# Kernel tuning notes

Hardware: AMD Instinct MI355X
Metric: run time of the kernel (lower is better)

Reference implementation:

```python
import jax, jax.numpy as jnp
import numpy as np

B, T, E = 2, 2048, 2048
H = 16
DH = E // H  # 128
FFN = 4 * E  # 8192
EPS = 1e-5


def _layernorm(x, g, b):
    mu = jnp.mean(x, axis=-1, keepdims=True)
    var = jnp.mean((x - mu) ** 2, axis=-1, keepdims=True)
    return (x - mu) * jax.lax.rsqrt(var + EPS) * g + b


def setup_inputs() -> dict:
    key = jax.random.key(0)
    ks = jax.random.split(key, 8)
    s = 0.02
    return {
        "x": jax.random.normal(ks[0], (B, T, E), jnp.float32),
        "g1": jnp.ones((E,), jnp.float32),
        "b1": jnp.zeros((E,), jnp.float32),
        "wq": jax.random.normal(ks[1], (E, E), jnp.float32) * s,
        "wk": jax.random.normal(ks[2], (E, E), jnp.float32) * s,
        "wv": jax.random.normal(ks[3], (E, E), jnp.float32) * s,
        "wo": jax.random.normal(ks[4], (E, E), jnp.float32) * s,
        "g2": jnp.ones((E,), jnp.float32),
        "b2": jnp.zeros((E,), jnp.float32),
        "w1": jax.random.normal(ks[5], (E, FFN), jnp.float32) * s,
        "w2": jax.random.normal(ks[6], (E, FFN), jnp.float32) * s,
        "w3": jax.random.normal(ks[7], (FFN, E), jnp.float32) * s,
    }


def reference(x, g1, b1, wq, wk, wv, wo, g2, b2, w1, w2, w3):
    Bx, Tx, Ex = x.shape
    # --- attention block (pre-LN, residual) ---
    h = _layernorm(x, g1, b1)
    q = (h @ wq).reshape(Bx, Tx, H, DH)
    k = (h @ wk).reshape(Bx, Tx, H, DH)
    v = (h @ wv).reshape(Bx, Tx, H, DH)
    scores = jnp.einsum('bqhd,bkhd->bhqk', q, k) / jnp.sqrt(jnp.float32(DH))
    causal = jnp.tril(jnp.ones((Tx, Tx), bool))  # [T,T]
    scores = jnp.where(causal[None, None], scores, -jnp.inf)
    attn = jax.nn.softmax(scores, axis=-1)
    ctx = jnp.einsum('bhqk,bkhd->bqhd', attn, v).reshape(Bx, Tx, H * DH)
    x = x + ctx @ wo
    # --- SwiGLU MLP block (pre-LN, residual) ---
    h = _layernorm(x, g2, b2)
    gated = jax.nn.silu(h @ w1) * (h @ w2)
    return x + gated @ w3
```

## Files before the change

kernel.cpp:

```cpp
#include <hip/hip_runtime.h>


#define T_SEQ 2048
#define E_DIM 2048
#define N_HEAD 16
#define D_HEAD 128
#define FFN_DIM 8192
#define M_ROWS 4096
#define QS (3 * E_DIM)

typedef unsigned short u16;
typedef short short8 __attribute__((ext_vector_type(8)));
typedef float f32x4 __attribute__((ext_vector_type(4)));

#define DEV __device__ __forceinline__

DEV u16 f2bf(float f) {
  unsigned u = __float_as_uint(f);
  u += 0x7fffu + ((u >> 16) & 1u);
  return (u16)(u >> 16);
}
DEV float bf2f(u16 h) { return __uint_as_float(((unsigned)h) << 16); }

DEV void async16(void* lds, const void* g) {
  __builtin_amdgcn_global_load_lds((const __attribute__((address_space(1))) void*)g,
                                   (__attribute__((address_space(3))) void*)lds, 16, 0, 0);
}

__global__ __launch_bounds__(256) void ln_kernel(const float* __restrict__ x,
                                                 const float* __restrict__ gw,
                                                 const float* __restrict__ bw,
                                                 u16* __restrict__ out) {
  int row = blockIdx.x;
  int t = threadIdx.x;
  const float4* xr = (const float4*)(x + (size_t)row * E_DIM);
  float4 a = xr[t], c = xr[t + 256];
  float s = a.x + a.y + a.z + a.w + c.x + c.y + c.z + c.w;
  float q = a.x * a.x + a.y * a.y + a.z * a.z + a.w * a.w +
            c.x * c.x + c.y * c.y + c.z * c.z + c.w * c.w;
  for (int off = 32; off > 0; off >>= 1) {
    s += __shfl_down(s, off);
    q += __shfl_down(q, off);
  }
  __shared__ float red[8];
  if ((t & 63) == 0) { red[(t >> 6) * 2] = s; red[(t >> 6) * 2 + 1] = q; }
  __syncthreads();
  s = red[0] + red[2] + red[4] + red[6];
  q = red[1] + red[3] + red[5] + red[7];
  float mu = s * (1.f / E_DIM);
  float rs = rsqrtf(q * (1.f / E_DIM) - mu * mu + 1e-5f);
  const float4* g4 = (const float4*)gw;
  const float4* b4 = (const float4*)bw;
  float4 g0 = g4[t], g1v = g4[t + 256], e0 = b4[t], e1 = b4[t + 256];
  ushort4 o0, o1;
  o0.x = f2bf((a.x - mu) * rs * g0.x + e0.x);
  o0.y = f2bf((a.y - mu) * rs * g0.y + e0.y);
  o0.z = f2bf((a.z - mu) * rs * g0.z + e0.z);
  o0.w = f2bf((a.w - mu) * rs * g0.w + e0.w);
  o1.x = f2bf((c.x - mu) * rs * g1v.x + e1.x);
  o1.y = f2bf((c.y - mu) * rs * g1v.y + e1.y);
  o1.z = f2bf((c.z - mu) * rs * g1v.z + e1.z);
  o1.w = f2bf((c.w - mu) * rs * g1v.w + e1.w);
  ((ushort4*)(out + (size_t)row * E_DIM))[t] = o0;
  ((ushort4*)(out + (size_t)row * E_DIM))[t + 256] = o1;
}

__global__ __launch_bounds__(256) void cvt_t_kernel(const float* __restrict__ W,
                                                    u16* __restrict__ WT,
                                                    int Kd, int Nd) {
  __shared__ float tile[32][33];
  int tx = threadIdx.x, ty = threadIdx.y;
  int n0 = blockIdx.x * 32, k0 = blockIdx.y * 32;
#pragma unroll
  for (int i = 0; i < 4; i++)
    tile[ty + i * 8][tx] = W[(size_t)(k0 + ty + i * 8) * Nd + n0 + tx];
  __syncthreads();
#pragma unroll
  for (int i = 0; i < 4; i++)
    WT[(size_t)(n0 + ty + i * 8) * Kd + k0 + tx] = f2bf(tile[tx][ty + i * 8]);
}

__global__ __launch_bounds__(256) void transpose_v_kernel(const u16* __restrict__ qkv,
                                                          u16* __restrict__ vt) {
  __shared__ u16 tile[32][33];
  int tx = threadIdx.x, ty = threadIdx.y;
  int b = blockIdx.z;
  int t0 = blockIdx.x * 32, e0 = blockIdx.y * 32;
#pragma unroll
  for (int i = 0; i < 4; i++)
    tile[ty + i * 8][tx] =
        qkv[(size_t)(b * T_SEQ + t0 + ty + i * 8) * QS + 2 * E_DIM + e0 + tx];
  __syncthreads();
#pragma unroll
  for (int i = 0; i < 4; i++)
    vt[((size_t)b * E_DIM + e0 + ty + i * 8) * T_SEQ + t0 + tx] = tile[tx][ty + i * 8];
}

template <int MODE, int BM_>
__global__ __launch_bounds__(512, 1) void gemm8p(const u16* __restrict__ A,
                                                 const u16* __restrict__ BT,
                                                 void* __restrict__ Cout,
                                                 const void* __restrict__ Extra,
                                                 int N, int K, int CX, int CY) {
  constexpr int MM = BM_ / 64;
  constexpr int AUNIT = BM_ * 32;
  __shared__ u16 Abuf[4 * AUNIT];
  __shared__ u16 Bbuf[4 * 8192];
  const int t = threadIdx.x;
  const int w = t >> 6, l = t & 63, g = l >> 4, lq = l & 15;
  const int wm = w >> 2, wn = w & 3;

  const int bid = blockIdx.y * gridDim.x + blockIdx.x;
  const int xcd = bid & 7, slot = bid >> 3;
  const int nchx = gridDim.x / CX;
  const int bx = (xcd % nchx) * CX + (slot % CX);
  const int by = (xcd / nchx) * CY + (slot / CX);
  const size_t bm = (size_t)by * BM_, bn = (size_t)bx * 256;

  const int srcrow = ((l >> 3) << 1) | (l & 1);
  const int csrc = ((((l >> 1) & 3) ^ ((l >> 3) & 3)) << 3);
  const u16* aSrc = A + (bm + w * 16 + srcrow) * (size_t)K + csrc;
  const u16* bSrc = BT + (bn + w * 16 + srcrow) * (size_t)K + csrc;
  const int rdoff = (((lq & 1) + 2 * (g ^ ((lq >> 1) & 3))) << 3);

#define STA8(DB, KS, TILE)                                                    \
  {                                                                           \
    u16* Ad = Abuf + (DB) * (2 * AUNIT) + (KS)*AUNIT + w * 512;               \
    const u16* as_ = aSrc + (size_t)(TILE)*64 + (KS)*32;                      \
    async16(Ad, as_);                                                         \
    if constexpr (BM_ == 256) async16(Ad + 4096, as_ + (size_t)128 * K);      \
  }
#define STB8(DB, KS, TILE)                                                    \
  {                                                                           \
    u16* Bd = Bbuf + (DB)*16384 + (KS)*8192 + w * 512;                        \
    const u16* bs_ = bSrc + (size_t)(TILE)*64 + (KS)*32;                      \
    async16(Bd, bs_);                                                         \
    async16(Bd + 4096, bs_ + (size_t)128 * K);                                \
  }
#define RDA8(DB, KS, MH)                                                      \
  _Pragma("unroll") for (int mm = 0; mm < MM; ++mm)                           \
      af[mm] = *(const short8*)(Abuf + (DB) * (2 * AUNIT) + (KS)*AUNIT +      \
                                (wm * (BM_ / 4) + (MH) * (BM_ / 8) + mm * 8 + \
                                 (lq >> 1)) * 64 + rdoff);
#define RDB8(DB, KS)                                                          \
  _Pragma("unroll") for (int nn = 0; nn < 4; ++nn)                            \
      bf[nn] = *(const short8*)(Bbuf + (DB)*16384 + (KS)*8192 +               \
                                (wn * 32 + nn * 8 + (lq >> 1)) * 64 + rdoff);
#define MM168(MH)                                                             \
  _Pragma("unroll") for (int mm = 0; mm < MM; ++mm)                           \
      _Pragma("unroll") for (int nn = 0; nn < 4; ++nn)                        \
          acc[(MH)*MM + mm][nn] = __builtin_amdgcn_mfma_f32_16x16x32_bf16(    \
              af[mm], bf[nn], acc[(MH)*MM + mm][nn], 0, 0, 0);
#define SYNCA                                                                 \
  __builtin_amdgcn_s_barrier();                                               \
  asm volatile("s_waitcnt lgkmcnt(0)" ::: "memory");                          \
  __builtin_amdgcn_sched_barrier(0);                                          \
  __builtin_amdgcn_s_setprio(1);
#define ENDP __builtin_amdgcn_s_setprio(0);
#define BAR2 __builtin_amdgcn_s_barrier();
#define WAITN                                                                 \
  if constexpr (BM_ == 256) asm volatile("s_waitcnt vmcnt(8)" ::: "memory");  \
  else                      asm volatile("s_waitcnt vmcnt(6)" ::: "memory");
#define WAITH                                                                 \
  if constexpr (BM_ == 256) asm volatile("s_waitcnt vmcnt(4)" ::: "memory");  \
  else                      asm volatile("s_waitcnt vmcnt(3)" ::: "memory");

  const int NT = K >> 6, NI = NT >> 1;
  f32x4 acc[2 * MM][4] = {};
  short8 af[MM > 4 ? MM : 4], bf[4];

  STA8(0, 0, 0); STB8(0, 0, 0);
  STA8(0, 1, 0); STB8(0, 1, 0);
  STA8(1, 0, 1); STB8(1, 0, 1);
  WAITN;
  BAR2;

  for (int j = 0; j < NI; ++j) {
    const int t1 = 2 * j + 1, t2 = 2 * j + 2, t3 = 2 * j + 3;
    const bool s2 = t2 < NT, s3 = t3 < NT, lastI = (j + 1 == NI);
    RDB8(0, 0); RDA8(0, 0, 0);
    STA8(1, 1, t1);
    SYNCA; MM168(0); ENDP; BAR2;
    RDA8(0, 0, 1);
    STB8(1, 1, t1);
    SYNCA; MM168(1); ENDP;
    WAITN;
    BAR2;
    RDB8(0, 1); RDA8(0, 1, 0);
    if (s2) STA8(0, 0, t2);
    SYNCA; MM168(0); ENDP; BAR2;
    RDA8(0, 1, 1);
    if (s2) STB8(0, 0, t2);
    SYNCA; MM168(1); ENDP;
    if (lastI) { WAITH; } else { WAITN; }
    BAR2;
    RDB8(1, 0); RDA8(1, 0, 0);
    if (s2) STA8(0, 1, t2);
    SYNCA; MM168(0); ENDP; BAR2;
    RDA8(1, 0, 1);
    if (s2) STB8(0, 1, t2);
    SYNCA; MM168(1); ENDP;
    if (lastI) { asm volatile("s_waitcnt vmcnt(0)" ::: "memory"); } else { WAITN; }
    BAR2;
    RDB8(1, 1); RDA8(1, 1, 0);
    if (s3) STA8(1, 0, t3);
    SYNCA; MM168(0); ENDP; BAR2;
    RDA8(1, 1, 1);
    if (s3) STB8(1, 0, t3);
    SYNCA; MM168(1); ENDP;
    if (!lastI) { WAITN; }
    BAR2;
  }
#undef STA8
#undef STB8
#undef RDA8
#undef RDB8
#undef MM168
#undef SYNCA
#undef ENDP
#undef BAR2
#undef WAITN
#undef WAITH

#pragma unroll
  for (int m = 0; m < 2 * MM; m++) {
    size_t row = bm + wm * (BM_ / 2) + m * 16 + 4 * g;
#pragma unroll
    for (int n = 0; n < 4; n++) {
      size_t col = bn + wn * 64 + n * 16 + lq;
#pragma unroll
      for (int r = 0; r < 4; r++) {
        size_t idx = (row + r) * (size_t)N + col;
        if constexpr (MODE == 0) {
          ((u16*)Cout)[idx] = f2bf(acc[m][n][r]);
        } else if constexpr (MODE == 1) {
          ((float*)Cout)[idx] = ((const float*)Extra)[idx] + acc[m][n][r];
        } else {
          float a = bf2f(((const u16*)Extra)[idx]);
          float sil = a / (1.f + exp2f(-1.4426950408889634f * a));
          ((u16*)Cout)[idx] = f2bf(sil * acc[m][n][r]);
        }
      }
    }
  }
}

__global__ __launch_bounds__(256, 3) void attn_kernel(const u16* __restrict__ QKV,
                                                      const u16* __restrict__ VT,
                                                      u16* __restrict__ CTX) {
  __shared__ u16 Ks[64 * 128];
  __shared__ u16 Vs[128 * 64];
  __shared__ u16 P_all[4][16 * 72];
  const int t = threadIdx.x;
  const int w = t >> 6, l = t & 63, g = l >> 4, lq = l & 15;
  u16* P = P_all[w];
  const int q0blk = blockIdx.x * 64;
  const int q0w = q0blk + w * 16;
  const int bh = blockIdx.y, b = bh >> 4, h = bh & 15;
  const u16* qp = QKV + (size_t)b * T_SEQ * QS + h * D_HEAD;
  const u16* kp = QKV + (size_t)b * T_SEQ * QS + E_DIM + h * D_HEAD;
  const u16* vp = VT + ((size_t)b * E_DIM + h * D_HEAD) * T_SEQ;

  short8 qf[4];
#pragma unroll
  for (int ks = 0; ks < 4; ks++)
    qf[ks] = *(const short8*)(qp + (size_t)(q0w + lq) * QS + ks * 32 + g * 8);

  f32x4 acc[8] = {};
  float m2[4], ls[4];
#pragma unroll
  for (int r = 0; r < 4; r++) { m2[r] = -1e30f; ls[r] = 0.f; }
  const float sc = 0.08838834764831845f * 1.4426950408889634f;

  const int kRow0 = 16 * w + (l >> 4);
  const int kChunk = l & 15;
  const int vRow0 = 32 * w + (l >> 3);
  const int vChunk = l & 7;

  for (int kv0 = 0; kv0 <= q0blk; kv0 += 64) {
#pragma unroll
    for (int j = 0; j < 4; j++) {
      int R = kRow0 + 4 * j;
      async16(Ks + (16 * w + 4 * j) * 128,
              kp + (size_t)(kv0 + R) * QS + ((kChunk ^ (R & 7)) << 3));
    }
#pragma unroll
    for (int j = 0; j < 4; j++) {
      int D = vRow0 + 8 * j;
      async16(Vs + (32 * w + 8 * j) * 64,
              vp + (size_t)D * T_SEQ + kv0 + ((vChunk ^ (D & 7)) << 3));
    }
    __syncthreads();

    f32x4 s[4];
#pragma unroll
    for (int ct = 0; ct < 4; ct++) {
      s[ct] = f32x4{0.f, 0.f, 0.f, 0.f};
#pragma unroll
      for (int ks = 0; ks < 4; ks++) {
        short8 kf = *(const short8*)(Ks + (ct * 16 + lq) * 128 +
                                     (((ks * 4 + g) ^ (lq & 7)) << 3));
        s[ct] = __builtin_amdgcn_mfma_f32_16x16x32_bf16(qf[ks], kf, s[ct], 0, 0, 0);
      }
    }
    float sv[4][4];
#pragma unroll
    for (int ct = 0; ct < 4; ct++)
#pragma unroll
      for (int r = 0; r < 4; r++) sv[ct][r] = s[ct][r] * sc;
    if (kv0 + 64 > q0w) {
#pragma unroll
      for (int ct = 0; ct < 4; ct++)
#pragma unroll
        for (int r = 0; r < 4; r++)
          if (kv0 + ct * 16 + lq > q0w + 4 * g + r) sv[ct][r] = -1e30f;
    }
    float mx[4];
#pragma unroll
    for (int r = 0; r < 4; r++)
      mx[r] = fmaxf(fmaxf(sv[0][r], sv[1][r]), fmaxf(sv[2][r], sv[3][r]));
#pragma unroll
    for (int off = 1; off < 16; off <<= 1)
#pragma unroll
      for (int r = 0; r < 4; r++) mx[r] = fmaxf(mx[r], __shfl_xor(mx[r], off));
#pragma unroll
    for (int r = 0; r < 4; r++) {
      float mn = fmaxf(m2[r], mx[r]);
      float sca = exp2f(m2[r] - mn);
      m2[r] = mn;
      float sum = 0.f;
#pragma unroll
      for (int ct = 0; ct < 4; ct++) {
        float pv = exp2f(sv[ct][r] - mn);
        sum += pv;
        P[(4 * g + r) * 72 + ct * 16 + lq] = f2bf(pv);
      }
      ls[r] = ls[r] * sca + sum;
#pragma unroll
      for (int n = 0; n < 8; n++) acc[n][r] *= sca;
    }
    short8 pa[2];
#pragma unroll
    for (int ks2 = 0; ks2 < 2; ks2++)
      pa[ks2] = *(const short8*)(P + lq * 72 + ks2 * 32 + g * 8);
#pragma unroll
    for (int n = 0; n < 8; n++)
#pragma unroll
      for (int ks2 = 0; ks2 < 2; ks2++) {
        short8 vf = *(const short8*)(Vs + (n * 16 + lq) * 64 +
                                     (((ks2 * 4 + g) ^ (lq & 7)) << 3));
        acc[n] = __builtin_amdgcn_mfma_f32_16x16x32_bf16(pa[ks2], vf, acc[n], 0, 0, 0);
      }
    __syncthreads();
  }

#pragma unroll
  for (int off = 1; off < 16; off <<= 1)
#pragma unroll
    for (int r = 0; r < 4; r++) ls[r] += __shfl_xor(ls[r], off);
  float inv[4];
#pragma unroll
  for (int r = 0; r < 4; r++) inv[r] = 1.f / ls[r];
  u16* cp = CTX + ((size_t)b * T_SEQ + q0w) * E_DIM + h * D_HEAD;
#pragma unroll
  for (int n = 0; n < 8; n++)
#pragma unroll
    for (int r = 0; r < 4; r++)
      cp[(size_t)(4 * g + r) * E_DIM + n * 16 + lq] = f2bf(acc[n][r] * inv[r]);
}

extern "C" void kernel_launch(void* const* d_in, const int* in_sizes, int n_in,
                              void* d_out, int out_size, void* d_ws, size_t ws_size,
                              hipStream_t stream) {
  (void)in_sizes; (void)n_in; (void)out_size; (void)ws_size;
  const float* x  = (const float*)d_in[0];
  const float* g1 = (const float*)d_in[1];
  const float* b1 = (const float*)d_in[2];
  const float* wq = (const float*)d_in[3];
  const float* wk = (const float*)d_in[4];
  const float* wv = (const float*)d_in[5];
  const float* wo = (const float*)d_in[6];
  const float* g2 = (const float*)d_in[7];
  const float* b2 = (const float*)d_in[8];
  const float* w1 = (const float*)d_in[9];
  const float* w2 = (const float*)d_in[10];
  const float* w3 = (const float*)d_in[11];
  float* out = (float*)d_out;

  const size_t EE2 = (size_t)E_DIM * E_DIM * 2;
  const size_t EF2 = (size_t)E_DIM * FFN_DIM * 2;
  const size_t ME2 = (size_t)M_ROWS * E_DIM * 2;
  char* p = (char*)d_ws;
  u16* wqkvT = (u16*)p; p += 3 * EE2;
  u16* woT = (u16*)p; p += EE2;
  u16* w1T = (u16*)p; p += EF2;
  u16* w2T = (u16*)p; p += EF2;
  u16* w3T = (u16*)p; p += EF2;
  u16* Hb  = (u16*)p; p += ME2;
  u16* QKVb = (u16*)p; p += (size_t)M_ROWS * QS * 2;
  u16* VTb = (u16*)p; p += ME2;
  u16* CTXb = (u16*)p; p += ME2;
  u16* U1b = QKVb;

  dim3 blk32(32, 8);
  cvt_t_kernel<<<dim3(E_DIM / 32, E_DIM / 32), blk32, 0, stream>>>(wq, wqkvT, E_DIM, E_DIM);
  cvt_t_kernel<<<dim3(E_DIM / 32, E_DIM / 32), blk32, 0, stream>>>(wk, wqkvT + E_DIM * E_DIM, E_DIM, E_DIM);
  cvt_t_kernel<<<dim3(E_DIM / 32, E_DIM / 32), blk32, 0, stream>>>(wv, wqkvT + 2 * E_DIM * E_DIM, E_DIM, E_DIM);
  cvt_t_kernel<<<dim3(E_DIM / 32, E_DIM / 32), blk32, 0, stream>>>(wo, woT, E_DIM, E_DIM);
  cvt_t_kernel<<<dim3(FFN_DIM / 32, E_DIM / 32), blk32, 0, stream>>>(w1, w1T, E_DIM, FFN_DIM);
  cvt_t_kernel<<<dim3(FFN_DIM / 32, E_DIM / 32), blk32, 0, stream>>>(w2, w2T, E_DIM, FFN_DIM);
  cvt_t_kernel<<<dim3(E_DIM / 32, FFN_DIM / 32), blk32, 0, stream>>>(w3, w3T, FFN_DIM, E_DIM);

  ln_kernel<<<M_ROWS, 256, 0, stream>>>(x, g1, b1, Hb);
  gemm8p<0, 128><<<dim3(QS / 256, M_ROWS / 128), 512, 0, stream>>>(Hb, wqkvT, QKVb, nullptr, QS, E_DIM, 6, 16);
  transpose_v_kernel<<<dim3(T_SEQ / 32, E_DIM / 32, 2), blk32, 0, stream>>>(QKVb, VTb);
  attn_kernel<<<dim3(T_SEQ / 64, 2 * N_HEAD), 256, 0, stream>>>(QKVb, VTb, CTXb);
  gemm8p<1, 128><<<dim3(E_DIM / 256, M_ROWS / 128), 512, 0, stream>>>(CTXb, woT, out, x, E_DIM, E_DIM, 4, 8);

  ln_kernel<<<M_ROWS, 256, 0, stream>>>(out, g2, b2, Hb);
  gemm8p<0, 256><<<dim3(FFN_DIM / 256, M_ROWS / 256), 512, 0, stream>>>(Hb, w1T, U1b, nullptr, FFN_DIM, E_DIM, 8, 8);
  gemm8p<2, 256><<<dim3(FFN_DIM / 256, M_ROWS / 256), 512, 0, stream>>>(Hb, w2T, U1b, U1b, FFN_DIM, E_DIM, 8, 8);
  gemm8p<1, 128><<<dim3(E_DIM / 256, M_ROWS / 128), 512, 0, stream>>>(U1b, w3T, out, out, E_DIM, FFN_DIM, 4, 8);
}
```

Measured before the change: 942.3 us.

## Split-K the down-projection GEMM and process 32 query rows per attention wave

The final FFN down-projection GEMM now uses 256-row tiles and a two-way split over K. Each half writes fp32 partials into the reused weight workspace, and a separate add kernel sums them into the residual output. This is meant to raise per-block work and parallelism for the long-K GEMM, at the cost of extra partial-sum memory traffic and one more launch. The attention kernel now handles 128 queries per block with two 16-row groups per wave, reusing each loaded K/V tile twice. It also adds MFMA priority hints and lowers occupancy to 2 blocks per CU.

```diff
diff --git a/kernel.cpp b/kernel.cpp
--- a/kernel.cpp
+++ b/kernel.cpp
@@ -96,12 +96,32 @@
     vt[((size_t)b * E_DIM + e0 + ty + i * 8) * T_SEQ + t0 + tx] = tile[tx][ty + i * 8];
 }
 
+__global__ __launch_bounds__(256) void add3_kernel(float* __restrict__ out,
+                                                   const float* __restrict__ pk) {
+  const size_t MN4 = (size_t)M_ROWS * E_DIM / 4;
+  size_t i = (size_t)blockIdx.x * 256 + threadIdx.x;
+  const float4* p04 = (const float4*)pk;
+  const float4* p14 = (const float4*)(pk + (size_t)M_ROWS * E_DIM);
+  float4* o4 = (float4*)out;
+#pragma unroll
+  for (int k = 0; k < 4; k++) {
+    size_t idx = i + (size_t)k * 524288;
+    if (idx < MN4) {
+      float4 o = o4[idx], a = p04[idx], b = p14[idx];
+      o.x += a.x + b.x; o.y += a.y + b.y;
+      o.z += a.z + b.z; o.w += a.w + b.w;
+      o4[idx] = o;
+    }
+  }
+}
+
 template <int MODE, int BM_>
 __global__ __launch_bounds__(512, 1) void gemm8p(const u16* __restrict__ A,
                                                  const u16* __restrict__ BT,
                                                  void* __restrict__ Cout,
                                                  const void* __restrict__ Extra,
-                                                 int N, int K, int CX, int CY) {
+                                                 int N, int K, int lda, int ldb,
+                                                 int CX, int CY) {
   constexpr int MM = BM_ / 64;
   constexpr int AUNIT = BM_ * 32;
   __shared__ u16 Abuf[4 * AUNIT];
@@ -110,17 +130,22 @@
   const int w = t >> 6, l = t & 63, g = l >> 4, lq = l & 15;
   const int wm = w >> 2, wn = w & 3;
 
-  const int bid = blockIdx.y * gridDim.x + blockIdx.x;
+  const int bid = (blockIdx.z * gridDim.y + blockIdx.y) * gridDim.x + blockIdx.x;
   const int xcd = bid & 7, slot = bid >> 3;
   const int nchx = gridDim.x / CX;
-  const int bx = (xcd % nchx) * CX + (slot % CX);
-  const int by = (xcd / nchx) * CY + (slot / CX);
+  const int nchy = gridDim.y / CY;
+  const int cpz = nchx * nchy;
+  const int kz = xcd / cpz;
+  const int cid = xcd % cpz;
+  const int bx = (cid % nchx) * CX + (slot % CX);
+  const int by = (cid / nchx) * CY + (slot / CX);
   const size_t bm = (size_t)by * BM_, bn = (size_t)bx * 256;
+  const size_t koff = (size_t)kz * K;
 
   const int srcrow = ((l >> 3) << 1) | (l & 1);
   const int csrc = ((((l >> 1) & 3) ^ ((l >> 3) & 3)) << 3);
-  const u16* aSrc = A + (bm + w * 16 + srcrow) * (size_t)K + csrc;
-  const u16* bSrc = BT + (bn + w * 16 + srcrow) * (size_t)K + csrc;
+  const u16* aSrc = A + (bm + w * 16 + srcrow) * (size_t)lda + koff + csrc;
+  const u16* bSrc = BT + (bn + w * 16 + srcrow) * (size_t)ldb + koff + csrc;
   const int rdoff = (((lq & 1) + 2 * (g ^ ((lq >> 1) & 3))) << 3);
 
 #define STA8(DB, KS, TILE)                                                    \
@@ -128,14 +153,14 @@
     u16* Ad = Abuf + (DB) * (2 * AUNIT) + (KS)*AUNIT + w * 512;               \
     const u16* as_ = aSrc + (size_t)(TILE)*64 + (KS)*32;                      \
     async16(Ad, as_);                                                         \
-    if constexpr (BM_ == 256) async16(Ad + 4096, as_ + (size_t)128 * K);      \
+    if constexpr (BM_ == 256) async16(Ad + 4096, as_ + (size_t)128 * lda);    \
   }
 #define STB8(DB, KS, TILE)                                                    \
   {                                                                           \
     u16* Bd = Bbuf + (DB)*16384 + (KS)*8192 + w * 512;                        \
     const u16* bs_ = bSrc + (size_t)(TILE)*64 + (KS)*32;                      \
     async16(Bd, bs_);                                                         \
-    async16(Bd + 4096, bs_ + (size_t)128 * K);                                \
+    async16(Bd + 4096, bs_ + (size_t)128 * ldb);                              \
   }
 #define RDA8(DB, KS, MH)                                                      \
   _Pragma("unroll") for (int mm = 0; mm < MM; ++mm)                           \
@@ -222,6 +247,7 @@
 #undef WAITN
 #undef WAITH
 
+  const size_t mn = (size_t)gridDim.y * BM_ * (size_t)N;
 #pragma unroll
   for (int m = 0; m < 2 * MM; m++) {
     size_t row = bm + wm * (BM_ / 2) + m * 16 + 4 * g;
@@ -235,41 +261,48 @@
           ((u16*)Cout)[idx] = f2bf(acc[m][n][r]);
         } else if constexpr (MODE == 1) {
           ((float*)Cout)[idx] = ((const float*)Extra)[idx] + acc[m][n][r];
-        } else {
+        } else if constexpr (MODE == 2) {
           float a = bf2f(((const u16*)Extra)[idx]);
           float sil = a / (1.f + exp2f(-1.4426950408889634f * a));
           ((u16*)Cout)[idx] = f2bf(sil * acc[m][n][r]);
+        } else {
+          ((float*)Cout)[(size_t)kz * mn + idx] = acc[m][n][r];
         }
       }
     }
   }
 }
 
-__global__ __launch_bounds__(256, 3) void attn_kernel(const u16* __restrict__ QKV,
+__global__ __launch_bounds__(256, 2) void attn_kernel(const u16* __restrict__ QKV,
                                                       const u16* __restrict__ VT,
                                                       u16* __restrict__ CTX) {
   __shared__ u16 Ks[64 * 128];
   __shared__ u16 Vs[128 * 64];
-  __shared__ u16 P_all[4][16 * 72];
+  __shared__ u16 P_all[4][32 * 72];
   const int t = threadIdx.x;
   const int w = t >> 6, l = t & 63, g = l >> 4, lq = l & 15;
   u16* P = P_all[w];
-  const int q0blk = blockIdx.x * 64;
-  const int q0w = q0blk + w * 16;
+  const int q0blk = blockIdx.x * 128;
+  const int q0w = q0blk + w * 32;
   const int bh = blockIdx.y, b = bh >> 4, h = bh & 15;
   const u16* qp = QKV + (size_t)b * T_SEQ * QS + h * D_HEAD;
   const u16* kp = QKV + (size_t)b * T_SEQ * QS + E_DIM + h * D_HEAD;
   const u16* vp = VT + ((size_t)b * E_DIM + h * D_HEAD) * T_SEQ;
 
-  short8 qf[4];
-#pragma unroll
-  for (int ks = 0; ks < 4; ks++)
-    qf[ks] = *(const short8*)(qp + (size_t)(q0w + lq) * QS + ks * 32 + g * 8);
-
-  f32x4 acc[8] = {};
-  float m2[4], ls[4];
-#pragma unroll
-  for (int r = 0; r < 4; r++) { m2[r] = -1e30f; ls[r] = 0.f; }
+  short8 qf[2][4];
+#pragma unroll
+  for (int rg = 0; rg < 2; rg++)
+#pragma unroll
+    for (int ks = 0; ks < 4; ks++)
+      qf[rg][ks] =
+          *(const short8*)(qp + (size_t)(q0w + rg * 16 + lq) * QS + ks * 32 + g * 8);
+
+  f32x4 acc[2][8] = {};
+  float m2[2][4], ls[2][4];
+#pragma unroll
+  for (int rg = 0; rg < 2; rg++)
+#pragma unroll
+    for (int r = 0; r < 4; r++) { m2[rg][r] = -1e30f; ls[rg][r] = 0.f; }
   const float sc = 0.08838834764831845f * 1.4426950408889634f;
 
   const int kRow0 = 16 * w + (l >> 4);
@@ -277,7 +310,7 @@
   const int vRow0 = 32 * w + (l >> 3);
   const int vChunk = l & 7;
 
-  for (int kv0 = 0; kv0 <= q0blk; kv0 += 64) {
+  for (int kv0 = 0; kv0 < q0blk + 128; kv0 += 64) {
 #pragma unroll
     for (int j = 0; j < 4; j++) {
       int R = kRow0 + 4 * j;
@@ -292,81 +325,97 @@
     }
     __syncthreads();
 
-    f32x4 s[4];
-#pragma unroll
-    for (int ct = 0; ct < 4; ct++) {
-      s[ct] = f32x4{0.f, 0.f, 0.f, 0.f};
-#pragma unroll
-      for (int ks = 0; ks < 4; ks++) {
-        short8 kf = *(const short8*)(Ks + (ct * 16 + lq) * 128 +
-                                     (((ks * 4 + g) ^ (lq & 7)) << 3));
-        s[ct] = __builtin_amdgcn_mfma_f32_16x16x32_bf16(qf[ks], kf, s[ct], 0, 0, 0);
+#pragma unroll
+    for (int rg = 0; rg < 2; rg++) {
+      const int rb = q0w + rg * 16;
+      if (kv0 > rb + 15) continue;
+      f32x4 s[4];
+      __builtin_amdgcn_s_setprio(1);
+#pragma unroll
+      for (int ct = 0; ct < 4; ct++) {
+        s[ct] = f32x4{0.f, 0.f, 0.f, 0.f};
+#pragma unroll
+        for (int ks = 0; ks < 4; ks++) {
+          short8 kf = *(const short8*)(Ks + (ct * 16 + lq) * 128 +
+                                       (((ks * 4 + g) ^ (lq & 7)) << 3));
+          s[ct] = __builtin_amdgcn_mfma_f32_16x16x32_bf16(qf[rg][ks], kf, s[ct], 0, 0, 0);
+        }
       }
+      __builtin_amdgcn_s_setprio(0);
+      float sv[4][4];
+#pragma unroll
+      for (int ct = 0; ct < 4; ct++)
+#pragma unroll
+        for (int r = 0; r < 4; r++) sv[ct][r] = s[ct][r] * sc;
+      if (kv0 + 64 > rb) {
+#pragma unroll
+        for (int ct = 0; ct < 4; ct++)
+#pragma unroll
+          for (int r = 0; r < 4; r++)
+            if (kv0 + ct * 16 + lq > rb + 4 * g + r) sv[ct][r] = -1e30f;
+      }
+      float mx[4];
+#pragma unroll
+      for (int r = 0; r < 4; r++)
+        mx[r] = fmaxf(fmaxf(sv[0][r], sv[1][r]), fmaxf(sv[2][r], sv[3][r]));
+#pragma unroll
+      for (int off = 1; off < 16; off <<= 1)
+#pragma unroll
+        for (int r = 0; r < 4; r++) mx[r] = fmaxf(mx[r], __shfl_xor(mx[r], off));
+#pragma unroll
+      for (int r = 0; r < 4; r++) {
+        float mn = fmaxf(m2[rg][r], mx[r]);
+        float sca = exp2f(m2[rg][r] - mn);
+        m2[rg][r] = mn;
+        float sum = 0.f;
+#pragma unroll
+        for (int ct = 0; ct < 4; ct++) {
+          float pv = exp2f(sv[ct][r] - mn);
+          sum += pv;
+          P[(rg * 16 + 4 * g + r) * 72 + ct * 16 + lq] = f2bf(pv);
+        }
+        ls[rg][r] = ls[rg][r] * sca + sum;
+#pragma unroll
+        for (int n = 0; n < 8; n++) acc[rg][n][r] *= sca;
+      }
+      short8 pa[2];
+#pragma unroll
+      for (int ks2 = 0; ks2 < 2; ks2++)
+        pa[ks2] = *(const short8*)(P + (rg * 16 + lq) * 72 + ks2 * 32 + g * 8);
+      __builtin_amdgcn_s_setprio(1);
+#pragma unroll
+      for (int n = 0; n < 8; n++)
+#pragma unroll
+        for (int ks2 = 0; ks2 < 2; ks2++) {
+          short8 vf = *(const short8*)(Vs + (n * 16 + lq) * 64 +
+                                       (((ks2 * 4 + g) ^ (lq & 7)) << 3));
+          acc[rg][n] = __builtin_amdgcn_mfma_f32_16x16x32_bf16(pa[ks2], vf, acc[rg][n], 0, 0, 0);
+        }
+      __builtin_amdgcn_s_setprio(0);
     }
-    float sv[4][4];
-#pragma unroll
-    for (int ct = 0; ct < 4; ct++)
-#pragma unroll
-      for (int r = 0; r < 4; r++) sv[ct][r] = s[ct][r] * sc;
-    if (kv0 + 64 > q0w) {
-#pragma unroll
-      for (int ct = 0; ct < 4; ct++)
-#pragma unroll
-        for (int r = 0; r < 4; r++)
-          if (kv0 + ct * 16 + lq > q0w + 4 * g + r) sv[ct][r] = -1e30f;
-    }
-    float mx[4];
-#pragma unroll
-    for (int r = 0; r < 4; r++)
-      mx[r] = fmaxf(fmaxf(sv[0][r], sv[1][r]), fmaxf(sv[2][r], sv[3][r]));
+    __syncthreads();
+  }
+
+#pragma unroll
+  for (int rg = 0; rg < 2; rg++) {
 #pragma unroll
     for (int off = 1; off < 16; off <<= 1)
 #pragma unroll
-      for (int r = 0; r < 4; r++) mx[r] = fmaxf(mx[r], __shfl_xor(mx[r], off));
-#pragma unroll
-    for (int r = 0; r < 4; r++) {
-      float mn = fmaxf(m2[r], mx[r]);
-      float sca = exp2f(m2[r] - mn);
-      m2[r] = mn;
-      float sum = 0.f;
-#pragma unroll
-      for (int ct = 0; ct < 4; ct++) {
-        float pv = exp2f(sv[ct][r] - mn);
-        sum += pv;
-        P[(4 * g + r) * 72 + ct * 16 + lq] = f2bf(pv);
-      }
-      ls[r] = ls[r] * sca + sum;
-#pragma unroll
-      for (int n = 0; n < 8; n++) acc[n][r] *= sca;
-    }
-    short8 pa[2];
-#pragma unroll
-    for (int ks2 = 0; ks2 < 2; ks2++)
-      pa[ks2] = *(const short8*)(P + lq * 72 + ks2 * 32 + g * 8);
+      for (int r = 0; r < 4; r++) ls[rg][r] += __shfl_xor(ls[rg][r], off);
+  }
+  u16* cp = CTX + ((size_t)b * T_SEQ + q0w) * E_DIM + h * D_HEAD;
+#pragma unroll
+  for (int rg = 0; rg < 2; rg++) {
+    float inv[4];
+#pragma unroll
+    for (int r = 0; r < 4; r++) inv[r] = 1.f / ls[rg][r];
 #pragma unroll
     for (int n = 0; n < 8; n++)
 #pragma unroll
-      for (int ks2 = 0; ks2 < 2; ks2++) {
-        short8 vf = *(const short8*)(Vs + (n * 16 + lq) * 64 +
-                                     (((ks2 * 4 + g) ^ (lq & 7)) << 3));
-        acc[n] = __builtin_amdgcn_mfma_f32_16x16x32_bf16(pa[ks2], vf, acc[n], 0, 0, 0);
-      }
-    __syncthreads();
-  }
-
-#pragma unroll
-  for (int off = 1; off < 16; off <<= 1)
-#pragma unroll
-    for (int r = 0; r < 4; r++) ls[r] += __shfl_xor(ls[r], off);
-  float inv[4];
-#pragma unroll
-  for (int r = 0; r < 4; r++) inv[r] = 1.f / ls[r];
-  u16* cp = CTX + ((size_t)b * T_SEQ + q0w) * E_DIM + h * D_HEAD;
-#pragma unroll
-  for (int n = 0; n < 8; n++)
-#pragma unroll
-    for (int r = 0; r < 4; r++)
-      cp[(size_t)(4 * g + r) * E_DIM + n * 16 + lq] = f2bf(acc[n][r] * inv[r]);
+      for (int r = 0; r < 4; r++)
+        cp[(size_t)(rg * 16 + 4 * g + r) * E_DIM + n * 16 + lq] =
+            f2bf(acc[rg][n][r] * inv[r]);
+  }
 }
 
 extern "C" void kernel_launch(void* const* d_in, const int* in_sizes, int n_in,
@@ -401,6 +450,7 @@
   u16* VTb = (u16*)p; p += ME2;
   u16* CTXb = (u16*)p; p += ME2;
   u16* U1b = QKVb;
+  float* Pk = (float*)wqkvT;
 
   dim3 blk32(32, 8);
   cvt_t_kernel<<<dim3(E_DIM / 32, E_DIM / 32), blk32, 0, stream>>>(wq, wqkvT, E_DIM, E_DIM);
@@ -412,13 +462,19 @@
   cvt_t_kernel<<<dim3(E_DIM / 32, FFN_DIM / 32), blk32, 0, stream>>>(w3, w3T, FFN_DIM, E_DIM);
 
   ln_kernel<<<M_ROWS, 256, 0, stream>>>(x, g1, b1, Hb);
-  gemm8p<0, 128><<<dim3(QS / 256, M_ROWS / 128), 512, 0, stream>>>(Hb, wqkvT, QKVb, nullptr, QS, E_DIM, 6, 16);
+  gemm8p<0, 128><<<dim3(QS / 256, M_ROWS / 128), 512, 0, stream>>>(
+      Hb, wqkvT, QKVb, nullptr, QS, E_DIM, E_DIM, E_DIM, 6, 16);
   transpose_v_kernel<<<dim3(T_SEQ / 32, E_DIM / 32, 2), blk32, 0, stream>>>(QKVb, VTb);
-  attn_kernel<<<dim3(T_SEQ / 64, 2 * N_HEAD), 256, 0, stream>>>(QKVb, VTb, CTXb);
-  gemm8p<1, 128><<<dim3(E_DIM / 256, M_ROWS / 128), 512, 0, stream>>>(CTXb, woT, out, x, E_DIM, E_DIM, 4, 8);
+  attn_kernel<<<dim3(T_SEQ / 128, 2 * N_HEAD), 256, 0, stream>>>(QKVb, VTb, CTXb);
+  gemm8p<1, 128><<<dim3(E_DIM / 256, M_ROWS / 128), 512, 0, stream>>>(
+      CTXb, woT, out, x, E_DIM, E_DIM, E_DIM, E_DIM, 4, 8);
 
   ln_kernel<<<M_ROWS, 256, 0, stream>>>(out, g2, b2, Hb);
-  gemm8p<0, 256><<<dim3(FFN_DIM / 256, M_ROWS / 256), 512, 0, stream>>>(Hb, w1T, U1b, nullptr, FFN_DIM, E_DIM, 8, 8);
-  gemm8p<2, 256><<<dim3(FFN_DIM / 256, M_ROWS / 256), 512, 0, stream>>>(Hb, w2T, U1b, U1b, FFN_DIM, E_DIM, 8, 8);
-  gemm8p<1, 128><<<dim3(E_DIM / 256, M_ROWS / 128), 512, 0, stream>>>(U1b, w3T, out, out, E_DIM, FFN_DIM, 4, 8);
-}
+  gemm8p<0, 256><<<dim3(FFN_DIM / 256, M_ROWS / 256), 512, 0, stream>>>(
+      Hb, w1T, U1b, nullptr, FFN_DIM, E_DIM, E_DIM, E_DIM, 8, 8);
+  gemm8p<2, 256><<<dim3(FFN_DIM / 256, M_ROWS / 256), 512, 0, stream>>>(
+      Hb, w2T, U1b, U1b, FFN_DIM, E_DIM, E_DIM, E_DIM, 8, 8);
+  gemm8p<3, 256><<<dim3(E_DIM / 256, M_ROWS / 256, 2), 512, 0, stream>>>(
+      U1b, w3T, Pk, nullptr, E_DIM, FFN_DIM / 2, FFN_DIM, FFN_DIM, 4, 8);
+  add3_kernel<<<2048, 256, 0, stream>>>(out, Pk);
+}
```

New measurement: 910.2 us. 3.4% less time.
